# Performance work log

Measured on AMD Instinct MI355X. Metric: run time of the kernel, lower is better.

Reference implementation:

```python
import jax, jax.numpy as jnp
import numpy as np

DT = 1.0       # integration timestep
THRESH = 0.5   # firing threshold (standard in this family of SNN repos)


def setup_inputs() -> dict:
    key = jax.random.key(0)
    ks = jax.random.split(key, 6)
    B, Din, Dout = 32768, 256, 512
    input_spike = jax.random.uniform(ks[0], (B, Din), dtype=jnp.float32)
    mem = jnp.zeros((B, Dout), jnp.float32)
    spike = jnp.zeros((B, Dout), jnp.float32)
    s_in = 1.0 / np.sqrt(Din)
    s_h = 1.0 / np.sqrt(Dout)
    W_dense = jax.random.uniform(ks[1], (Dout, Din), minval=-s_in, maxval=s_in, dtype=jnp.float32)
    b_dense = jax.random.uniform(ks[2], (Dout,), minval=-s_in, maxval=s_in, dtype=jnp.float32)
    W_rec = jax.random.uniform(ks[3], (Dout, Dout), minval=-s_h, maxval=s_h, dtype=jnp.float32)
    b_rec = jax.random.uniform(ks[4], (Dout,), minval=-s_h, maxval=s_h, dtype=jnp.float32)
    tau_m = 20.0 + 5.0 * jax.random.normal(ks[5], (Dout,), dtype=jnp.float32)
    return dict(input_spike=input_spike, mem=mem, spike=spike,
                W_dense=W_dense, b_dense=b_dense, W_rec=W_rec, b_rec=b_rec,
                tau_m=tau_m)


def reference(input_spike, mem, spike, W_dense, b_dense, W_rec, b_rec, tau_m):
    # d_input = dense(input_spike) + recurrent(spike)
    d_input = (jnp.einsum('bi,oi->bo', input_spike, W_dense) + b_dense
               + jnp.einsum('bh,oh->bo', spike, W_rec) + b_rec)
    # LIF neuron dynamics: exponential membrane decay, soft reset, heaviside spike
    alpha = jnp.exp(-DT / tau_m)                                   # [Dout]
    mem_new = mem * alpha + (1.0 - alpha) * d_input - THRESH * spike
    spike_new = (mem_new - THRESH > 0).astype(mem_new.dtype)
    return mem_new, spike_new
```

## Files before the change

kernel.cpp:

```cpp
#include <hip/hip_runtime.h>
#include <math.h>

typedef short  short8  __attribute__((ext_vector_type(8)));
typedef short  short4v __attribute__((ext_vector_type(4)));
typedef float  f32x4   __attribute__((ext_vector_type(4)));

#define BATCH 32768
#define DIN   256
#define DOUT  512
#define BM    128
#define BN    64

#define WS_FLAGS 0
#define WS_WD2   4096
#define WS_WR2   (4096 + 262144)
#define WS_X2    (266240 + 524288)

__device__ __forceinline__ short f2bf(float v) {
    unsigned u = __float_as_uint(v);
    u += 0x7fffu + ((u >> 16) & 1u);
    return (short)(u >> 16);
}

__device__ __forceinline__ void gload_lds16(const void* g, void* l) {
    __builtin_amdgcn_global_load_lds(
        (const __attribute__((address_space(1))) unsigned int*)g,
        (__attribute__((address_space(3))) unsigned int*)l, 16, 0, 0);
}

__global__ __launch_bounds__(256) void prepass_kernel(
    const float* __restrict__ SPK, const float* __restrict__ X,
    const float* __restrict__ Wd,  const float* __restrict__ Wr,
    int* __restrict__ flags, short* __restrict__ X2,
    short* __restrict__ Wd2, short* __restrict__ Wr2)
{
    const int b   = blockIdx.x;
    const int tid = threadIdx.x;

    {
        unsigned bits = 0;
        const f32x4* p = (const f32x4*)SPK + (size_t)b * 2048;
#pragma unroll
        for (int j = 0; j < 8; j++) {
            f32x4 v = p[tid + j * 256];
            bits |= __float_as_uint(v[0]) | __float_as_uint(v[1])
                  | __float_as_uint(v[2]) | __float_as_uint(v[3]);
        }
        if (__any(bits != 0) && (tid & 63) == 0)
            atomicOr(&flags[b >> 3], 1);
    }

    {
        const f32x4* src = (const f32x4*)X + (size_t)b * 1024;
        short4v*     dst = (short4v*)X2   + (size_t)b * 1024;
#pragma unroll
        for (int j = 0; j < 4; j++) {
            f32x4 v = src[tid + j * 256];
            dst[tid + j * 256] = (short4v){f2bf(v[0]), f2bf(v[1]),
                                           f2bf(v[2]), f2bf(v[3])};
        }
    }

    {
        int idx = b * 256 + tid;
        if (idx < 32768) {
            f32x4 v = ((const f32x4*)Wd)[idx];
            ((short4v*)Wd2)[idx] = (short4v){f2bf(v[0]), f2bf(v[1]),
                                             f2bf(v[2]), f2bf(v[3])};
        } else if (idx < 98304) {
            int k = idx - 32768;
            f32x4 v = ((const f32x4*)Wr)[k];
            ((short4v*)Wr2)[k] = (short4v){f2bf(v[0]), f2bf(v[1]),
                                           f2bf(v[2]), f2bf(v[3])};
        }
    }
}

__global__ __launch_bounds__(256, 3) void spike_rnn_lif_kernel(
    const short* __restrict__ X2,
    const float* __restrict__ MEM,
    const float* __restrict__ SPK,
    const short* __restrict__ Wd2,
    const float* __restrict__ bd,
    const short* __restrict__ Wr2,
    const float* __restrict__ br,
    const float* __restrict__ tau,
    const int*   __restrict__ flags,
    float* __restrict__ out)
{
    __shared__ __align__(16) char smem[49152];
    float* sT = (float*)smem;

    const int tid  = threadIdx.x;
    const int lane = tid & 63;
    const int w    = tid >> 6;
    const int wm   = w & 1;
    const int wn   = w >> 1;

    const int L    = blockIdx.x;
    const int bm   = ((L >> 6) << 3) + (L & 7);
    const int bn   = (L >> 3) & 7;
    const int m0   = bm * BM;
    const int n0   = bn * BN;
    const int col  = lane & 15;
    const int quad = lane >> 4;

    const bool has_spk = (flags[bm] != 0);

    const int l16 = lane & 15, lr4 = lane >> 4;

#define STAGE(c0)                                                             \
    do {                                                                      \
        _Pragma("unroll")                                                     \
        for (int i = 0; i < 8; i++) {                                         \
            int seg = w * 8 + i;                     \
            int r   = seg * 4 + lr4;                                          \
            const char* src = (const char*)X2 + (size_t)(m0 + r) * 512        \
                            + (c0) * 256 + ((l16 * 16) ^ ((r & 7) << 4));     \
            gload_lds16(src, smem + seg * 1024);                              \
        }                                                                     \
        _Pragma("unroll")                                                     \
        for (int i = 0; i < 4; i++) {                                         \
            int seg = w * 4 + i;                                              \
            int r   = seg * 4 + lr4;                                          \
            const char* src = (const char*)Wd2 + (size_t)(n0 + r) * 512       \
                            + (c0) * 256 + ((l16 * 16) ^ ((r & 7) << 4));     \
            gload_lds16(src, smem + 32768 + seg * 1024);                      \
        }                                                                     \
    } while (0)

    STAGE(0);

    const int c4   = tid & 15;
    const int ncol = n0 + c4 * 4;
    f32x4 mv0[4], mv1[4];
#pragma unroll
    for (int it = 0; it < 4; it++) {
        int r2 = (tid + it * 256) >> 4;
        mv0[it] = __builtin_nontemporal_load(
                      (const f32x4*)(MEM + (size_t)(m0 + r2) * DOUT + ncol));
        mv1[it] = __builtin_nontemporal_load(
                      (const f32x4*)(MEM + (size_t)(m0 + 64 + r2) * DOUT + ncol));
    }

    f32x4 acc[4][2];
#pragma unroll
    for (int i = 0; i < 4; i++)
#pragma unroll
        for (int j = 0; j < 2; j++)
            acc[i][j] = (f32x4){0.f, 0.f, 0.f, 0.f};

    const int swz  = (col & 7) << 4;
    const int arow = wm * 64 + col;
    const int brow = wn * 32 + col;

#define DSLOAD(kk, aa, bb)                                                    \
    do {                                                                      \
        int ko = (quad * 16 + (kk) * 64) ^ swz;                               \
        _Pragma("unroll")                                                     \
        for (int t = 0; t < 4; t++)                                           \
            aa[t] = *(const short8*)(smem + (arow + t * 16) * 256 + ko);      \
        _Pragma("unroll")                                                     \
        for (int t = 0; t < 2; t++)                                           \
            bb[t] = *(const short8*)(smem + 32768 + (brow + t * 16) * 256 + ko); \
    } while (0)

#define MFMA_AB(aa, bb)                                                       \
    do {                                                                      \
        _Pragma("unroll")                                                     \
        for (int i = 0; i < 4; i++)                                           \
            _Pragma("unroll")                                                 \
            for (int j = 0; j < 2; j++)                                       \
                acc[i][j] = __builtin_amdgcn_mfma_f32_16x16x32_bf16(          \
                    aa[i], bb[j], acc[i][j], 0, 0, 0);                        \
    } while (0)

    short8 a0[4], b0[2], a1[4], b1[2];

    __syncthreads();
    DSLOAD(0, a0, b0);
    DSLOAD(1, a1, b1); MFMA_AB(a0, b0);
    DSLOAD(2, a0, b0); MFMA_AB(a1, b1);
    DSLOAD(3, a1, b1); MFMA_AB(a0, b0);
    MFMA_AB(a1, b1);
    __syncthreads();

    STAGE(1);
    __syncthreads();
    DSLOAD(0, a0, b0);
    DSLOAD(1, a1, b1); MFMA_AB(a0, b0);
    DSLOAD(2, a0, b0); MFMA_AB(a1, b1);
    DSLOAD(3, a1, b1); MFMA_AB(a0, b0);
    MFMA_AB(a1, b1);
#undef DSLOAD
#undef STAGE

    if (has_spk) {
        const float* Abase = SPK + (size_t)(m0 + wm * 64 + col) * DOUT + quad * 8;
        const short* Bbase = Wr2 + (size_t)(n0 + wn * 32 + col) * DOUT + quad * 8;
#pragma unroll 4
        for (int ks = 0; ks < 16; ks++) {
            int k = ks * 32;
            short8 a[4], b[2];
#pragma unroll
            for (int t = 0; t < 4; t++) {
                const float* ap = Abase + (size_t)t * 16 * DOUT + k;
                f32x4 lo = *(const f32x4*)ap;
                f32x4 hi = *(const f32x4*)(ap + 4);
                a[t] = (short8){f2bf(lo[0]), f2bf(lo[1]), f2bf(lo[2]), f2bf(lo[3]),
                                f2bf(hi[0]), f2bf(hi[1]), f2bf(hi[2]), f2bf(hi[3])};
            }
#pragma unroll
            for (int t = 0; t < 2; t++)
                b[t] = *(const short8*)(Bbase + (size_t)t * 16 * DOUT + k);
            MFMA_AB(a, b);
        }
    }
#undef MFMA_AB

    float al[4], oma[4], bs[4];
#pragma unroll
    for (int q = 0; q < 4; q++) {
        al[q]  = expf(-1.0f / tau[ncol + q]);
        oma[q] = 1.0f - al[q];
        bs[q]  = bd[ncol + q] + br[ncol + q];
    }

    __syncthreads();

#pragma unroll
    for (int c = 0; c < 2; c++) {
        if (c) __syncthreads();
        if (wm == c) {
#pragma unroll
            for (int j = 0; j < 2; j++)
#pragma unroll
                for (int i = 0; i < 4; i++)
#pragma unroll
                    for (int rr = 0; rr < 4; rr++)
                        sT[(i * 16 + quad * 4 + rr) * 68 + wn * 32 + j * 16 + col]
                            = acc[i][j][rr];
        }
        __syncthreads();
#pragma unroll
        for (int it = 0; it < 4; it++) {
            int p   = tid + it * 256;
            int r2  = p >> 4;
            int row = m0 + c * 64 + r2;
            f32x4 d  = *(const f32x4*)(sT + r2 * 68 + c4 * 4);
            f32x4 mv = c ? mv1[it] : mv0[it];
            f32x4 sv = has_spk ? *(const f32x4*)(SPK + (size_t)row * DOUT + ncol)
                               : (f32x4){0.f, 0.f, 0.f, 0.f};
            f32x4 mn, sp;
#pragma unroll
            for (int q = 0; q < 4; q++) {
                mn[q] = mv[q] * al[q] + oma[q] * (d[q] + bs[q]) - 0.5f * sv[q];
                sp[q] = (mn[q] - 0.5f > 0.0f) ? 1.0f : 0.0f;
            }
            __builtin_nontemporal_store(mn,
                (f32x4*)(out + (size_t)row * DOUT + ncol));
            __builtin_nontemporal_store(sp,
                (f32x4*)(out + (size_t)BATCH * DOUT + (size_t)row * DOUT + ncol));
        }
    }
}

extern "C" void kernel_launch(void* const* d_in, const int* in_sizes, int n_in,
                              void* d_out, int out_size, void* d_ws, size_t ws_size,
                              hipStream_t stream) {
    const float* X   = (const float*)d_in[0];
    const float* MEM = (const float*)d_in[1];
    const float* SPK = (const float*)d_in[2];
    const float* Wd  = (const float*)d_in[3];
    const float* bd  = (const float*)d_in[4];
    const float* Wr  = (const float*)d_in[5];
    const float* br  = (const float*)d_in[6];
    const float* tau = (const float*)d_in[7];

    char*  ws    = (char*)d_ws;
    int*   flags = (int*)  (ws + WS_FLAGS);
    short* Wd2   = (short*)(ws + WS_WD2);
    short* Wr2   = (short*)(ws + WS_WR2);
    short* X2    = (short*)(ws + WS_X2);

    hipMemsetAsync(flags, 0, 256 * sizeof(int), stream);
    prepass_kernel<<<2048, 256, 0, stream>>>(SPK, X, Wd, Wr, flags, X2, Wd2, Wr2);

    spike_rnn_lif_kernel<<<2048, 256, 0, stream>>>(X2, MEM, SPK, Wd2, bd, Wr2, br,
                                                   tau, flags, (float*)d_out);
}
```

Baseline: 272.6 us.

## Double-buffer dense-GEMM LDS staging in four K-chunks with prefetch

```diff
diff --git a/kernel.cpp b/kernel.cpp
--- a/kernel.cpp
+++ b/kernel.cpp
@@ -107,29 +107,27 @@
 
     const bool has_spk = (flags[bm] != 0);
 
-    const int l16 = lane & 15, lr4 = lane >> 4;
-
-#define STAGE(c0)                                                             \
+#define STAGE(c0, buf)                                                        \
     do {                                                                      \
-        _Pragma("unroll")                                                     \
-        for (int i = 0; i < 8; i++) {                                         \
-            int seg = w * 8 + i;                     \
-            int r   = seg * 4 + lr4;                                          \
-            const char* src = (const char*)X2 + (size_t)(m0 + r) * 512        \
-                            + (c0) * 256 + ((l16 * 16) ^ ((r & 7) << 4));     \
-            gload_lds16(src, smem + seg * 1024);                              \
-        }                                                                     \
         _Pragma("unroll")                                                     \
         for (int i = 0; i < 4; i++) {                                         \
             int seg = w * 4 + i;                                              \
-            int r   = seg * 4 + lr4;                                          \
+            int r   = seg * 8 + (lane >> 3);                                  \
+            const char* src = (const char*)X2 + (size_t)(m0 + r) * 512        \
+                + (c0) * 128 + (((lane & 7) * 16) ^ ((r & 7) << 4));          \
+            gload_lds16(src, (buf) + seg * 1024);                             \
+        }                                                                     \
+        _Pragma("unroll")                                                     \
+        for (int i = 0; i < 2; i++) {                                         \
+            int seg = w * 2 + i;                                              \
+            int r   = seg * 8 + (lane >> 3);                                  \
             const char* src = (const char*)Wd2 + (size_t)(n0 + r) * 512       \
-                            + (c0) * 256 + ((l16 * 16) ^ ((r & 7) << 4));     \
-            gload_lds16(src, smem + 32768 + seg * 1024);                      \
+                + (c0) * 128 + (((lane & 7) * 16) ^ ((r & 7) << 4));          \
+            gload_lds16(src, (buf) + 16384 + seg * 1024);                     \
         }                                                                     \
     } while (0)
 
-    STAGE(0);
+    STAGE(0, smem);
 
     const int c4   = tid & 15;
     const int ncol = n0 + c4 * 4;
@@ -154,15 +152,15 @@
     const int arow = wm * 64 + col;
     const int brow = wn * 32 + col;
 
-#define DSLOAD(kk, aa, bb)                                                    \
+#define DSLOAD(buf, kk, aa, bb)                                               \
     do {                                                                      \
         int ko = (quad * 16 + (kk) * 64) ^ swz;                               \
         _Pragma("unroll")                                                     \
         for (int t = 0; t < 4; t++)                                           \
-            aa[t] = *(const short8*)(smem + (arow + t * 16) * 256 + ko);      \
+            aa[t] = *(const short8*)((buf) + (arow + t * 16) * 128 + ko);     \
         _Pragma("unroll")                                                     \
         for (int t = 0; t < 2; t++)                                           \
-            bb[t] = *(const short8*)(smem + 32768 + (brow + t * 16) * 256 + ko); \
+            bb[t] = *(const short8*)((buf) + 16384 + (brow + t * 16) * 128 + ko); \
     } while (0)
 
 #define MFMA_AB(aa, bb)                                                       \
@@ -178,20 +176,19 @@
     short8 a0[4], b0[2], a1[4], b1[2];
 
     __syncthreads();
-    DSLOAD(0, a0, b0);
-    DSLOAD(1, a1, b1); MFMA_AB(a0, b0);
-    DSLOAD(2, a0, b0); MFMA_AB(a1, b1);
-    DSLOAD(3, a1, b1); MFMA_AB(a0, b0);
-    MFMA_AB(a1, b1);
-    __syncthreads();
-
-    STAGE(1);
-    __syncthreads();
-    DSLOAD(0, a0, b0);
-    DSLOAD(1, a1, b1); MFMA_AB(a0, b0);
-    DSLOAD(2, a0, b0); MFMA_AB(a1, b1);
-    DSLOAD(3, a1, b1); MFMA_AB(a0, b0);
-    MFMA_AB(a1, b1);
+#pragma unroll
+    for (int c = 0; c < 4; c++) {
+        char* cur = smem + (c & 1) * 24576;
+        if (c < 3) {
+            char* nxt = smem + ((c + 1) & 1) * 24576;
+            STAGE(c + 1, nxt);
+        }
+        DSLOAD(cur, 0, a0, b0);
+        DSLOAD(cur, 1, a1, b1);
+        MFMA_AB(a0, b0);
+        MFMA_AB(a1, b1);
+        if (c < 3) __syncthreads();
+    }
 #undef DSLOAD
 #undef STAGE
 
@@ -225,8 +222,6 @@
         oma[q] = 1.0f - al[q];
         bs[q]  = bd[ncol + q] + br[ncol + q];
     }
-
-    __syncthreads();
 
 #pragma unroll
     for (int c = 0; c < 2; c++) {
```

Measured after the change: 274.9 us. About the same (+0.9%).

## Drop bf16 prepass and convert fp32 operands to bf16 inside the GEMM kernel

Applied to the files above, without the earlier changes.

```diff
diff --git a/kernel.cpp b/kernel.cpp
--- a/kernel.cpp
+++ b/kernel.cpp
@@ -2,7 +2,6 @@
 #include <math.h>
 
 typedef short  short8  __attribute__((ext_vector_type(8)));
-typedef short  short4v __attribute__((ext_vector_type(4)));
 typedef float  f32x4   __attribute__((ext_vector_type(4)));
 
 #define BATCH 32768
@@ -11,11 +10,6 @@
 #define BM    128
 #define BN    64
 
-#define WS_FLAGS 0
-#define WS_WD2   4096
-#define WS_WR2   (4096 + 262144)
-#define WS_X2    (266240 + 524288)
-
 __device__ __forceinline__ short f2bf(float v) {
     unsigned u = __float_as_uint(v);
     u += 0x7fffu + ((u >> 16) & 1u);
@@ -28,61 +22,30 @@
         (__attribute__((address_space(3))) unsigned int*)l, 16, 0, 0);
 }
 
-__global__ __launch_bounds__(256) void prepass_kernel(
-    const float* __restrict__ SPK, const float* __restrict__ X,
-    const float* __restrict__ Wd,  const float* __restrict__ Wr,
-    int* __restrict__ flags, short* __restrict__ X2,
-    short* __restrict__ Wd2, short* __restrict__ Wr2)
+__global__ __launch_bounds__(256) void scan_kernel(
+    const float* __restrict__ SPK, int* __restrict__ flags)
 {
     const int b   = blockIdx.x;
     const int tid = threadIdx.x;
-
-    {
-        unsigned bits = 0;
-        const f32x4* p = (const f32x4*)SPK + (size_t)b * 2048;
-#pragma unroll
-        for (int j = 0; j < 8; j++) {
-            f32x4 v = p[tid + j * 256];
-            bits |= __float_as_uint(v[0]) | __float_as_uint(v[1])
-                  | __float_as_uint(v[2]) | __float_as_uint(v[3]);
-        }
-        if (__any(bits != 0) && (tid & 63) == 0)
-            atomicOr(&flags[b >> 3], 1);
-    }
-
-    {
-        const f32x4* src = (const f32x4*)X + (size_t)b * 1024;
-        short4v*     dst = (short4v*)X2   + (size_t)b * 1024;
-#pragma unroll
-        for (int j = 0; j < 4; j++) {
-            f32x4 v = src[tid + j * 256];
-            dst[tid + j * 256] = (short4v){f2bf(v[0]), f2bf(v[1]),
-                                           f2bf(v[2]), f2bf(v[3])};
-        }
-    }
-
-    {
-        int idx = b * 256 + tid;
-        if (idx < 32768) {
-            f32x4 v = ((const f32x4*)Wd)[idx];
-            ((short4v*)Wd2)[idx] = (short4v){f2bf(v[0]), f2bf(v[1]),
-                                             f2bf(v[2]), f2bf(v[3])};
-        } else if (idx < 98304) {
-            int k = idx - 32768;
-            f32x4 v = ((const f32x4*)Wr)[k];
-            ((short4v*)Wr2)[k] = (short4v){f2bf(v[0]), f2bf(v[1]),
-                                           f2bf(v[2]), f2bf(v[3])};
-        }
-    }
+    unsigned bits = 0;
+    const f32x4* p = (const f32x4*)SPK + (size_t)b * 2048;
+#pragma unroll
+    for (int j = 0; j < 8; j++) {
+        f32x4 v = p[tid + j * 256];
+        bits |= __float_as_uint(v[0]) | __float_as_uint(v[1])
+              | __float_as_uint(v[2]) | __float_as_uint(v[3]);
+    }
+    if (__any(bits != 0) && (tid & 63) == 0)
+        atomicOr(&flags[b >> 3], 1);
 }
 
 __global__ __launch_bounds__(256, 3) void spike_rnn_lif_kernel(
-    const short* __restrict__ X2,
+    const float* __restrict__ X,
     const float* __restrict__ MEM,
     const float* __restrict__ SPK,
-    const short* __restrict__ Wd2,
+    const float* __restrict__ Wd,
     const float* __restrict__ bd,
-    const short* __restrict__ Wr2,
+    const float* __restrict__ Wr,
     const float* __restrict__ br,
     const float* __restrict__ tau,
     const int*   __restrict__ flags,
@@ -107,24 +70,22 @@
 
     const bool has_spk = (flags[bm] != 0);
 
-    const int l16 = lane & 15, lr4 = lane >> 4;
-
 #define STAGE(c0)                                                             \
     do {                                                                      \
         _Pragma("unroll")                                                     \
         for (int i = 0; i < 8; i++) {                                         \
-            int seg = w * 8 + i;                     \
-            int r   = seg * 4 + lr4;                                          \
-            const char* src = (const char*)X2 + (size_t)(m0 + r) * 512        \
-                            + (c0) * 256 + ((l16 * 16) ^ ((r & 7) << 4));     \
+            int seg = w * 8 + i;                                              \
+            int r   = seg * 4 + (lane >> 4);                                  \
+            const char* src = (const char*)X + (size_t)(m0 + r) * 1024        \
+                + (c0) * 256 + (((lane & 15) * 16) ^ ((r & 7) << 4));         \
             gload_lds16(src, smem + seg * 1024);                              \
         }                                                                     \
         _Pragma("unroll")                                                     \
         for (int i = 0; i < 4; i++) {                                         \
             int seg = w * 4 + i;                                              \
-            int r   = seg * 4 + lr4;                                          \
-            const char* src = (const char*)Wd2 + (size_t)(n0 + r) * 512       \
-                            + (c0) * 256 + ((l16 * 16) ^ ((r & 7) << 4));     \
+            int r   = seg * 4 + (lane >> 4);                                  \
+            const char* src = (const char*)Wd + (size_t)(n0 + r) * 1024       \
+                + (c0) * 256 + (((lane & 15) * 16) ^ ((r & 7) << 4));         \
             gload_lds16(src, smem + 32768 + seg * 1024);                      \
         }                                                                     \
     } while (0)
@@ -154,15 +115,23 @@
     const int arow = wm * 64 + col;
     const int brow = wn * 32 + col;
 
+#define PACK8(base, o0, dst)                                                  \
+    do {                                                                      \
+        f32x4 lo_ = *(const f32x4*)((base) + (((o0)     ) ^ swz));            \
+        f32x4 hi_ = *(const f32x4*)((base) + (((o0) + 16) ^ swz));            \
+        dst = (short8){f2bf(lo_[0]), f2bf(lo_[1]), f2bf(lo_[2]), f2bf(lo_[3]),\
+                       f2bf(hi_[0]), f2bf(hi_[1]), f2bf(hi_[2]), f2bf(hi_[3])};\
+    } while (0)
+
 #define DSLOAD(kk, aa, bb)                                                    \
     do {                                                                      \
-        int ko = (quad * 16 + (kk) * 64) ^ swz;                               \
+        int o0 = (kk) * 128 + quad * 32;                                      \
         _Pragma("unroll")                                                     \
         for (int t = 0; t < 4; t++)                                           \
-            aa[t] = *(const short8*)(smem + (arow + t * 16) * 256 + ko);      \
+            PACK8(smem + (size_t)(arow + t * 16) * 256, o0, aa[t]);           \
         _Pragma("unroll")                                                     \
         for (int t = 0; t < 2; t++)                                           \
-            bb[t] = *(const short8*)(smem + 32768 + (brow + t * 16) * 256 + ko); \
+            PACK8(smem + 32768 + (size_t)(brow + t * 16) * 256, o0, bb[t]);   \
     } while (0)
 
 #define MFMA_AB(aa, bb)                                                       \
@@ -178,26 +147,24 @@
     short8 a0[4], b0[2], a1[4], b1[2];
 
     __syncthreads();
-    DSLOAD(0, a0, b0);
-    DSLOAD(1, a1, b1); MFMA_AB(a0, b0);
-    DSLOAD(2, a0, b0); MFMA_AB(a1, b1);
-    DSLOAD(3, a1, b1); MFMA_AB(a0, b0);
-    MFMA_AB(a1, b1);
-    __syncthreads();
-
-    STAGE(1);
-    __syncthreads();
-    DSLOAD(0, a0, b0);
-    DSLOAD(1, a1, b1); MFMA_AB(a0, b0);
-    DSLOAD(2, a0, b0); MFMA_AB(a1, b1);
-    DSLOAD(3, a1, b1); MFMA_AB(a0, b0);
-    MFMA_AB(a1, b1);
+#pragma unroll
+    for (int c = 0; c < 4; c++) {
+        DSLOAD(0, a0, b0);
+        DSLOAD(1, a1, b1);
+        MFMA_AB(a0, b0);
+        MFMA_AB(a1, b1);
+        if (c < 3) {
+            __syncthreads();
+            STAGE(c + 1);
+            __syncthreads();
+        }
+    }
 #undef DSLOAD
 #undef STAGE
 
     if (has_spk) {
         const float* Abase = SPK + (size_t)(m0 + wm * 64 + col) * DOUT + quad * 8;
-        const short* Bbase = Wr2 + (size_t)(n0 + wn * 32 + col) * DOUT + quad * 8;
+        const float* Bbase = Wr  + (size_t)(n0 + wn * 32 + col) * DOUT + quad * 8;
 #pragma unroll 4
         for (int ks = 0; ks < 16; ks++) {
             int k = ks * 32;
@@ -211,12 +178,18 @@
                                 f2bf(hi[0]), f2bf(hi[1]), f2bf(hi[2]), f2bf(hi[3])};
             }
 #pragma unroll
-            for (int t = 0; t < 2; t++)
-                b[t] = *(const short8*)(Bbase + (size_t)t * 16 * DOUT + k);
+            for (int t = 0; t < 2; t++) {
+                const float* bp = Bbase + (size_t)t * 16 * DOUT + k;
+                f32x4 lo = *(const f32x4*)bp;
+                f32x4 hi = *(const f32x4*)(bp + 4);
+                b[t] = (short8){f2bf(lo[0]), f2bf(lo[1]), f2bf(lo[2]), f2bf(lo[3]),
+                                f2bf(hi[0]), f2bf(hi[1]), f2bf(hi[2]), f2bf(hi[3])};
+            }
             MFMA_AB(a, b);
         }
     }
 #undef MFMA_AB
+#undef PACK8
 
     float al[4], oma[4], bs[4];
 #pragma unroll
@@ -277,15 +250,11 @@
     const float* br  = (const float*)d_in[6];
     const float* tau = (const float*)d_in[7];
 
-    char*  ws    = (char*)d_ws;
-    int*   flags = (int*)  (ws + WS_FLAGS);
-    short* Wd2   = (short*)(ws + WS_WD2);
-    short* Wr2   = (short*)(ws + WS_WR2);
-    short* X2    = (short*)(ws + WS_X2);
+    int* flags = (int*)d_ws;
 
     hipMemsetAsync(flags, 0, 256 * sizeof(int), stream);
-    prepass_kernel<<<2048, 256, 0, stream>>>(SPK, X, Wd, Wr, flags, X2, Wd2, Wr2);
-
-    spike_rnn_lif_kernel<<<2048, 256, 0, stream>>>(X2, MEM, SPK, Wd2, bd, Wr2, br,
+    scan_kernel<<<2048, 256, 0, stream>>>(SPK, flags);
+
+    spike_rnn_lif_kernel<<<2048, 256, 0, stream>>>(X, MEM, SPK, Wd, bd, Wr, br,
                                                    tau, flags, (float*)d_out);
 }
```

Result: slower. 304.5 us (+11.7%).
